# Kernel tuning notes

Hardware: AMD Instinct MI355X
Metric: run time of the kernel (lower is better)

## Reference

```python
import jax, jax.numpy as jnp
import numpy as np

N = 50000      # nodes
E = 1000000    # edges
D = 64         # in_dim == out_dim
R = 200        # num_rels


def setup_inputs() -> dict:
    key = jax.random.key(0)
    ks = jax.random.split(key, 11)
    return {
        "n_feats": jax.random.normal(ks[0], (N, D), jnp.float32),
        "r_feats": jax.random.normal(ks[1], (R, D), jnp.float32),
        "W_I_w": jax.random.normal(ks[2], (D, D), jnp.float32) * 0.1,
        "W_I_b": jax.random.normal(ks[3], (D,), jnp.float32) * 0.1,
        "W_O_w": jax.random.normal(ks[4], (D, D), jnp.float32) * 0.1,
        "W_O_b": jax.random.normal(ks[5], (D,), jnp.float32) * 0.1,
        "W_R_w": jax.random.normal(ks[6], (D, D), jnp.float32) * 0.1,
        "W_R_b": jax.random.normal(ks[7], (D,), jnp.float32) * 0.1,
        "src": jax.random.randint(ks[8], (E,), 0, N),
        "dst": jax.random.randint(ks[9], (E,), 0, N),
        "etype": jax.random.randint(ks[10], (E,), 0, R),
        "num_rels": R,
    }


def reference(n_feats, r_feats, W_I_w, W_I_b, W_O_w, W_O_b, W_R_w, W_R_b,
              src, dst, etype, num_rels):
    # per-edge composition (comp_fn='sub'): h_src - r[etype]   [E, D]
    comp_h = n_feats[src] - r_feats[etype]
    # conditional linear per edge: W_I for etype < num_rels//2, else W_O
    h_i = comp_h @ W_I_w.T + W_I_b
    h_o = comp_h @ W_O_w.T + W_O_b
    mask = (etype < num_rels // 2)[:, None]
    new_comp_h = jnp.where(mask, h_i, h_o)
    # segment-mean scatter to destination nodes (DGL fn.mean)
    num_nodes = n_feats.shape[0]
    seg_sum = jax.ops.segment_sum(new_comp_h, dst, num_segments=num_nodes)
    deg = jax.ops.segment_sum(jnp.ones((new_comp_h.shape[0],), new_comp_h.dtype),
                              dst, num_segments=num_nodes)
    n_out_feats = seg_sum / jnp.maximum(deg, 1.0)[:, None]
    # dropout in eval mode = identity; no batchnorm, no activation, no self-loop
    r_out_feats = r_feats @ W_R_w.T + W_R_b
    return n_out_feats, r_out_feats
```

## Files before the change

kernel.cpp:

```cpp
#include <hip/hip_runtime.h>


#define DIM 64
#define NPB 8
#define WPAD 68
#define NBUCK 256
#define EPB 4096
#define CAP 8192

__device__ __forceinline__ unsigned int pack_bf16(float2 v) {
    unsigned int a = __float_as_uint(v.x);
    unsigned int b = __float_as_uint(v.y);
    a = (a + 0x7FFFu + ((a >> 16) & 1u)) >> 16;
    b = (b + 0x7FFFu + ((b >> 16) & 1u)) >> 16;
    return (a & 0xFFFFu) | (b << 16);
}

__global__ __launch_bounds__(256) void cvt_kernel(
    const float* __restrict__ n_feats, const float* __restrict__ r_feats,
    unsigned int* __restrict__ nfb, unsigned int* __restrict__ rfb,
    int nN2, int nR2)
{
    int i = blockIdx.x * blockDim.x + threadIdx.x;
    if (i < nN2) {
        nfb[i] = pack_bf16(((const float2*)n_feats)[i]);
    } else if (i < nN2 + nR2) {
        int k = i - nN2;
        rfb[k] = pack_bf16(((const float2*)r_feats)[k]);
    }
}

__global__ __launch_bounds__(512) void scatter_kernel(
    const int* __restrict__ src, const int* __restrict__ dst,
    const int* __restrict__ etype, int* __restrict__ bcur,
    unsigned int* __restrict__ es, int E)
{
    __shared__ int cnt[NBUCK];
    __shared__ int loff[NBUCK];
    __shared__ int woff[NBUCK];
    __shared__ int lold[NBUCK];
    __shared__ unsigned int stg[EPB];

    int tid = threadIdx.x;
    int base = blockIdx.x * EPB;
    int end = min(base + EPB, E);
    int m = end - base;

    if (tid < NBUCK) cnt[tid] = 0;
    __syncthreads();

    unsigned int val[8];
    int bk[8];
    #pragma unroll
    for (int k = 0; k < 8; ++k) {
        int e = base + tid + k * 512;
        if (e < end) {
            unsigned int d = (unsigned)dst[e];
            bk[k] = (int)(d >> 8);
            val[k] = ((d & 255u) << 24) | (((unsigned)src[e]) << 8)
                   | (unsigned)etype[e];
            atomicAdd(&cnt[bk[k]], 1);
        } else {
            bk[k] = -1;
            val[k] = 0u;
        }
    }
    __syncthreads();

    if (tid < NBUCK) loff[tid] = cnt[tid];
    __syncthreads();
    for (int off = 1; off < NBUCK; off <<= 1) {
        int t = 0;
        if (tid < NBUCK && tid >= off) t = loff[tid - off];
        __syncthreads();
        if (tid < NBUCK) loff[tid] += t;
        __syncthreads();
    }
    if (tid < NBUCK) {
        int excl = loff[tid] - cnt[tid];
        woff[tid] = excl;
        lold[tid] = (cnt[tid] > 0) ? atomicAdd(&bcur[tid], cnt[tid]) : 0;
    }
    __syncthreads();

    #pragma unroll
    for (int k = 0; k < 8; ++k) {
        if (bk[k] >= 0) {
            int p = atomicAdd(&woff[bk[k]], 1);
            stg[p] = val[k];
        }
    }
    __syncthreads();

    for (int j = tid; j < m; j += 512) {
        int lo_ = 0, hi_ = NBUCK;
        while (lo_ < hi_) {
            int mid = (lo_ + hi_) >> 1;
            if (loff[mid] > j) hi_ = mid; else lo_ = mid + 1;
        }
        int b = lo_;
        int excl = loff[b] - cnt[b];
        int local = lold[b] + (j - excl);
        if (local < CAP) es[(size_t)b * CAP + local] = stg[j];
    }
}

__global__ __launch_bounds__(512) void bsort_kernel(
    const unsigned int* __restrict__ es, const int* __restrict__ bcur,
    unsigned int* __restrict__ es2, int* __restrict__ rowptr,
    int* __restrict__ deg, int* __restrict__ degI,
    const int* __restrict__ num_rels, int N)
{
    __shared__ int nd[512], nl[512], ncur[512];

    int b = blockIdx.x, tid = threadIdx.x;
    int base = b * CAP;
    int cnt = min(bcur[b], CAP);
    int half = num_rels[0] >> 1;

    nd[tid] = 0;
    __syncthreads();
    for (int j = tid; j < cnt; j += 512) {
        unsigned int e = es[base + j];
        int k = (int)((e >> 24) << 1) | ((int)(e & 0xFFu) >= half ? 1 : 0);
        atomicAdd(&nd[k], 1);
    }
    __syncthreads();

    nl[tid] = nd[tid];
    __syncthreads();
    for (int off = 1; off < 512; off <<= 1) {
        int t = (tid >= off) ? nl[tid - off] : 0;
        __syncthreads();
        nl[tid] += t;
        __syncthreads();
    }
    ncur[tid] = nl[tid] - nd[tid];
    if ((tid & 1) == 0) {
        int v = (b << 8) + (tid >> 1);
        if (v < N) {
            rowptr[v] = base + (nl[tid] - nd[tid]);
            degI[v]   = nd[tid];
            deg[v]    = nd[tid] + nd[tid + 1];
        }
    }
    __syncthreads();

    for (int j = tid; j < cnt; j += 512) {
        unsigned int e = es[base + j];
        int k = (int)((e >> 24) << 1) | ((int)(e & 0xFFu) >= half ? 1 : 0);
        int p = atomicAdd(&ncur[k], 1);
        es2[base + p] = e;
    }
}

__device__ __forceinline__ void acc8(const uint4 f, const uint4 r, float* a) {
    a[0] += __uint_as_float(f.x << 16)         - __uint_as_float(r.x << 16);
    a[1] += __uint_as_float(f.x & 0xFFFF0000u) - __uint_as_float(r.x & 0xFFFF0000u);
    a[2] += __uint_as_float(f.y << 16)         - __uint_as_float(r.y << 16);
    a[3] += __uint_as_float(f.y & 0xFFFF0000u) - __uint_as_float(r.y & 0xFFFF0000u);
    a[4] += __uint_as_float(f.z << 16)         - __uint_as_float(r.z << 16);
    a[5] += __uint_as_float(f.z & 0xFFFF0000u) - __uint_as_float(r.z & 0xFFFF0000u);
    a[6] += __uint_as_float(f.w << 16)         - __uint_as_float(r.w << 16);
    a[7] += __uint_as_float(f.w & 0xFFFF0000u) - __uint_as_float(r.w & 0xFFFF0000u);
}

#define EDGE_LOOP(BND, A)                                              \
    for (; i + 8 < (BND); i += 16) {                                   \
        unsigned int ea = es2[i], eb = es2[i + 8];                     \
        uint4 fa = nf4[(size_t)((ea >> 8) & 0xFFFFu) * 8 + fl];        \
        uint4 ra = rf4[(size_t)(ea & 0xFFu) * 8 + fl];                 \
        uint4 fb = nf4[(size_t)((eb >> 8) & 0xFFFFu) * 8 + fl];        \
        uint4 rb = rf4[(size_t)(eb & 0xFFu) * 8 + fl];                 \
        acc8(fa, ra, A);                                               \
        acc8(fb, rb, A);                                               \
    }                                                                  \
    for (; i < (BND); i += 8) {                                        \
        unsigned int ea = es2[i];                                      \
        uint4 fa = nf4[(size_t)((ea >> 8) & 0xFFFFu) * 8 + fl];        \
        uint4 ra = rf4[(size_t)(ea & 0xFFu) * 8 + fl];                 \
        acc8(fa, ra, A);                                               \
    }

__global__ __launch_bounds__(512, 4) void rows_kernel(
    const unsigned int* __restrict__ nfb, const unsigned int* __restrict__ rfb,
    const float* __restrict__ r_feats,
    const int* __restrict__ rowptr, const int* __restrict__ degs,
    const int* __restrict__ degIs, const unsigned int* __restrict__ es2,
    const float* __restrict__ W_I_w, const float* __restrict__ W_I_b,
    const float* __restrict__ W_O_w, const float* __restrict__ W_O_b,
    const float* __restrict__ W_R_w, const float* __restrict__ W_R_b,
    float* __restrict__ n_out, float* __restrict__ r_out, int N, int Rr)
{
    __shared__ float WIp[DIM * WPAD];
    __shared__ float WOp[DIM * WPAD];
    __shared__ float xI[NPB][DIM];
    __shared__ float xO[NPB][DIM];

    const int tid = threadIdx.x;
    for (int i = tid; i < DIM * DIM; i += 512) {
        int j = i >> 6, d = i & 63;
        WIp[j * WPAD + d] = W_I_w[i];
        WOp[j * WPAD + d] = W_O_w[i];
    }
    __syncthreads();

    const int wv = tid >> 6, lane = tid & 63;
    const int e8 = lane >> 3, fl = lane & 7;
    const uint4* nf4 = (const uint4*)nfb;
    const uint4* rf4 = (const uint4*)rfb;

    int row = blockIdx.x * NPB + wv;
    if (row < N) {
        int lo = rowptr[row];
        int dI = degIs[row];
        int dT = degs[row];
        int mid = lo + dI, hi = lo + dT;
        float aI[8] = {0.f, 0.f, 0.f, 0.f, 0.f, 0.f, 0.f, 0.f};
        float aO[8] = {0.f, 0.f, 0.f, 0.f, 0.f, 0.f, 0.f, 0.f};

        int i = lo + e8;
        EDGE_LOOP(mid, aI);
        i = mid + e8;
        EDGE_LOOP(hi, aO);

        #pragma unroll
        for (int d = 8; d < 64; d <<= 1) {
            #pragma unroll
            for (int k = 0; k < 8; ++k) {
                aI[k] += __shfl_xor(aI[k], d, 64);
                aO[k] += __shfl_xor(aO[k], d, 64);
            }
        }
        if (e8 == 0) {
            #pragma unroll
            for (int k = 0; k < 8; ++k) {
                xI[wv][fl * 8 + k] = aI[k];
                xO[wv][fl * 8 + k] = aO[k];
            }
        }

        float sum = (float)dI * W_I_b[lane] + (float)(dT - dI) * W_O_b[lane];
        #pragma unroll
        for (int d4 = 0; d4 < DIM; d4 += 4) {
            float4 wi = *(const float4*)&WIp[lane * WPAD + d4];
            float4 wo = *(const float4*)&WOp[lane * WPAD + d4];
            float4 xi = *(const float4*)&xI[wv][d4];
            float4 xo = *(const float4*)&xO[wv][d4];
            sum += wi.x*xi.x + wi.y*xi.y + wi.z*xi.z + wi.w*xi.w
                 + wo.x*xo.x + wo.y*xo.y + wo.z*xo.z + wo.w*xo.w;
        }
        __builtin_nontemporal_store(sum / (float)(dT > 1 ? dT : 1),
                                    &n_out[(size_t)row * DIM + lane]);
    } else if (row < N + Rr) {
        int r = row - N;
        const float4* wr4 = (const float4*)W_R_w;
        const float4* rr4 = (const float4*)r_feats;
        float sum = W_R_b[lane];
        #pragma unroll
        for (int d4 = 0; d4 < 16; ++d4) {
            float4 w = wr4[(size_t)lane * 16 + d4];
            float4 x = rr4[(size_t)r * 16 + d4];
            sum += w.x*x.x + w.y*x.y + w.z*x.z + w.w*x.w;
        }
        __builtin_nontemporal_store(sum, &r_out[(size_t)r * DIM + lane]);
    }
}

extern "C" void kernel_launch(void* const* d_in, const int* in_sizes, int n_in,
                              void* d_out, int out_size, void* d_ws, size_t ws_size,
                              hipStream_t stream) {
    const float* n_feats  = (const float*)d_in[0];
    const float* r_feats  = (const float*)d_in[1];
    const float* W_I_w    = (const float*)d_in[2];
    const float* W_I_b    = (const float*)d_in[3];
    const float* W_O_w    = (const float*)d_in[4];
    const float* W_O_b    = (const float*)d_in[5];
    const float* W_R_w    = (const float*)d_in[6];
    const float* W_R_b    = (const float*)d_in[7];
    const int*   src      = (const int*)d_in[8];
    const int*   dst      = (const int*)d_in[9];
    const int*   etype    = (const int*)d_in[10];
    const int*   num_rels = (const int*)d_in[11];

    const int N  = in_sizes[0] / DIM;
    const int Rr = in_sizes[1] / DIM;
    const int E  = in_sizes[8];

    unsigned int* es   = (unsigned int*)d_ws;
    unsigned int* es2  = es + (size_t)NBUCK * CAP;
    unsigned int* nfb  = es2 + (size_t)NBUCK * CAP;
    unsigned int* rfb  = nfb + (size_t)N * (DIM / 2);
    int* bcur   = (int*)(rfb + (size_t)Rr * (DIM / 2));
    int* rowptr = bcur + NBUCK;
    int* deg    = rowptr + N;
    int* degI   = deg + N;

    float* n_out = (float*)d_out;
    float* r_out = n_out + (size_t)N * DIM;

    hipMemsetAsync(bcur, 0, NBUCK * sizeof(int), stream);

    int nN2 = N * (DIM / 2), nR2 = Rr * (DIM / 2);
    cvt_kernel<<<(nN2 + nR2 + 255) / 256, 256, 0, stream>>>(
        n_feats, r_feats, nfb, rfb, nN2, nR2);

    int sb = (E + EPB - 1) / EPB;
    scatter_kernel<<<sb, 512, 0, stream>>>(src, dst, etype, bcur, es, E);

    int nbUsed = (N + 255) >> 8;
    bsort_kernel<<<nbUsed, 512, 0, stream>>>(
        es, bcur, es2, rowptr, deg, degI, num_rels, N);

    int rowsBlocks = (N + Rr + NPB - 1) / NPB;
    rows_kernel<<<rowsBlocks, 512, 0, stream>>>(
        nfb, rfb, r_feats, rowptr, deg, degI, es2,
        W_I_w, W_I_b, W_O_w, W_O_b, W_R_w, W_R_b,
        n_out, r_out, N, Rr);
}
```

Baseline: 192.9 us.

## Fuse conversion into scatter launch, stage bucket in LDS, merge I/O edge loops

The bf16 conversion kernel is folded into the scatter kernel as extra blocks, so one launch covers both and the two independent jobs can overlap. The bucket sort now loads each bucket into shared memory once instead of reading global memory twice. The rows kernel replaces its two separate edge loops (I half and O half) with one loop that keeps a total sum and a masked I sum, then derives the O sum as the difference. This removes per-row loop overhead and the tail imbalance, but adds an FMA per element, and the subtraction can change rounding. The conversion blocks also carry the scatter kernel's large shared-memory footprint, which may lower their occupancy.

```diff
diff --git a/kernel.cpp b/kernel.cpp
--- a/kernel.cpp
+++ b/kernel.cpp
@@ -16,24 +16,13 @@
     return (a & 0xFFFFu) | (b << 16);
 }
 
-__global__ __launch_bounds__(256) void cvt_kernel(
+__global__ __launch_bounds__(512) void build_kernel(
+    const int* __restrict__ src, const int* __restrict__ dst,
+    const int* __restrict__ etype, int* __restrict__ bcur,
+    unsigned int* __restrict__ es, int E, int sb,
     const float* __restrict__ n_feats, const float* __restrict__ r_feats,
     unsigned int* __restrict__ nfb, unsigned int* __restrict__ rfb,
     int nN2, int nR2)
-{
-    int i = blockIdx.x * blockDim.x + threadIdx.x;
-    if (i < nN2) {
-        nfb[i] = pack_bf16(((const float2*)n_feats)[i]);
-    } else if (i < nN2 + nR2) {
-        int k = i - nN2;
-        rfb[k] = pack_bf16(((const float2*)r_feats)[k]);
-    }
-}
-
-__global__ __launch_bounds__(512) void scatter_kernel(
-    const int* __restrict__ src, const int* __restrict__ dst,
-    const int* __restrict__ etype, int* __restrict__ bcur,
-    unsigned int* __restrict__ es, int E)
 {
     __shared__ int cnt[NBUCK];
     __shared__ int loff[NBUCK];
@@ -42,6 +31,18 @@
     __shared__ unsigned int stg[EPB];
 
     int tid = threadIdx.x;
+
+    if (blockIdx.x >= sb) {
+        int i = (blockIdx.x - sb) * 512 + tid;
+        if (i < nN2) {
+            nfb[i] = pack_bf16(((const float2*)n_feats)[i]);
+        } else if (i < nN2 + nR2) {
+            int k = i - nN2;
+            rfb[k] = pack_bf16(((const float2*)r_feats)[k]);
+        }
+        return;
+    }
+
     int base = blockIdx.x * EPB;
     int end = min(base + EPB, E);
     int m = end - base;
@@ -111,6 +112,7 @@
     int* __restrict__ deg, int* __restrict__ degI,
     const int* __restrict__ num_rels, int N)
 {
+    __shared__ unsigned int st[CAP];
     __shared__ int nd[512], nl[512], ncur[512];
 
     int b = blockIdx.x, tid = threadIdx.x;
@@ -119,9 +121,11 @@
     int half = num_rels[0] >> 1;
 
     nd[tid] = 0;
-    __syncthreads();
+    for (int j = tid; j < cnt; j += 512) st[j] = es[base + j];
+    __syncthreads();
+
     for (int j = tid; j < cnt; j += 512) {
-        unsigned int e = es[base + j];
+        unsigned int e = st[j];
         int k = (int)((e >> 24) << 1) | ((int)(e & 0xFFu) >= half ? 1 : 0);
         atomicAdd(&nd[k], 1);
     }
@@ -147,40 +151,33 @@
     __syncthreads();
 
     for (int j = tid; j < cnt; j += 512) {
-        unsigned int e = es[base + j];
+        unsigned int e = st[j];
         int k = (int)((e >> 24) << 1) | ((int)(e & 0xFFu) >= half ? 1 : 0);
         int p = atomicAdd(&ncur[k], 1);
         es2[base + p] = e;
     }
 }
 
-__device__ __forceinline__ void acc8(const uint4 f, const uint4 r, float* a) {
-    a[0] += __uint_as_float(f.x << 16)         - __uint_as_float(r.x << 16);
-    a[1] += __uint_as_float(f.x & 0xFFFF0000u) - __uint_as_float(r.x & 0xFFFF0000u);
-    a[2] += __uint_as_float(f.y << 16)         - __uint_as_float(r.y << 16);
-    a[3] += __uint_as_float(f.y & 0xFFFF0000u) - __uint_as_float(r.y & 0xFFFF0000u);
-    a[4] += __uint_as_float(f.z << 16)         - __uint_as_float(r.z << 16);
-    a[5] += __uint_as_float(f.z & 0xFFFF0000u) - __uint_as_float(r.z & 0xFFFF0000u);
-    a[6] += __uint_as_float(f.w << 16)         - __uint_as_float(r.w << 16);
-    a[7] += __uint_as_float(f.w & 0xFFFF0000u) - __uint_as_float(r.w & 0xFFFF0000u);
-}
-
-#define EDGE_LOOP(BND, A)                                              \
-    for (; i + 8 < (BND); i += 16) {                                   \
-        unsigned int ea = es2[i], eb = es2[i + 8];                     \
-        uint4 fa = nf4[(size_t)((ea >> 8) & 0xFFFFu) * 8 + fl];        \
-        uint4 ra = rf4[(size_t)(ea & 0xFFu) * 8 + fl];                 \
-        uint4 fb = nf4[(size_t)((eb >> 8) & 0xFFFFu) * 8 + fl];        \
-        uint4 rb = rf4[(size_t)(eb & 0xFFu) * 8 + fl];                 \
-        acc8(fa, ra, A);                                               \
-        acc8(fb, rb, A);                                               \
-    }                                                                  \
-    for (; i < (BND); i += 8) {                                        \
-        unsigned int ea = es2[i];                                      \
-        uint4 fa = nf4[(size_t)((ea >> 8) & 0xFFFFu) * 8 + fl];        \
-        uint4 ra = rf4[(size_t)(ea & 0xFFu) * 8 + fl];                 \
-        acc8(fa, ra, A);                                               \
-    }
+__device__ __forceinline__ void acc8m(const uint4 f, const uint4 r, float w,
+                                      float* aT, float* aI) {
+    float c;
+    c = __uint_as_float(f.x << 16)         - __uint_as_float(r.x << 16);
+    aT[0] += c; aI[0] = fmaf(w, c, aI[0]);
+    c = __uint_as_float(f.x & 0xFFFF0000u) - __uint_as_float(r.x & 0xFFFF0000u);
+    aT[1] += c; aI[1] = fmaf(w, c, aI[1]);
+    c = __uint_as_float(f.y << 16)         - __uint_as_float(r.y << 16);
+    aT[2] += c; aI[2] = fmaf(w, c, aI[2]);
+    c = __uint_as_float(f.y & 0xFFFF0000u) - __uint_as_float(r.y & 0xFFFF0000u);
+    aT[3] += c; aI[3] = fmaf(w, c, aI[3]);
+    c = __uint_as_float(f.z << 16)         - __uint_as_float(r.z << 16);
+    aT[4] += c; aI[4] = fmaf(w, c, aI[4]);
+    c = __uint_as_float(f.z & 0xFFFF0000u) - __uint_as_float(r.z & 0xFFFF0000u);
+    aT[5] += c; aI[5] = fmaf(w, c, aI[5]);
+    c = __uint_as_float(f.w << 16)         - __uint_as_float(r.w << 16);
+    aT[6] += c; aI[6] = fmaf(w, c, aI[6]);
+    c = __uint_as_float(f.w & 0xFFFF0000u) - __uint_as_float(r.w & 0xFFFF0000u);
+    aT[7] += c; aI[7] = fmaf(w, c, aI[7]);
+}
 
 __global__ __launch_bounds__(512, 4) void rows_kernel(
     const unsigned int* __restrict__ nfb, const unsigned int* __restrict__ rfb,
@@ -217,26 +214,41 @@
         int dT = degs[row];
         int mid = lo + dI, hi = lo + dT;
         float aI[8] = {0.f, 0.f, 0.f, 0.f, 0.f, 0.f, 0.f, 0.f};
-        float aO[8] = {0.f, 0.f, 0.f, 0.f, 0.f, 0.f, 0.f, 0.f};
+        float aT[8] = {0.f, 0.f, 0.f, 0.f, 0.f, 0.f, 0.f, 0.f};
 
         int i = lo + e8;
-        EDGE_LOOP(mid, aI);
-        i = mid + e8;
-        EDGE_LOOP(hi, aO);
+        for (; i + 8 < hi; i += 16) {
+            unsigned int ea = es2[i], eb = es2[i + 8];
+            uint4 fa = nf4[(size_t)((ea >> 8) & 0xFFFFu) * 8 + fl];
+            uint4 ra = rf4[(size_t)(ea & 0xFFu) * 8 + fl];
+            uint4 fb = nf4[(size_t)((eb >> 8) & 0xFFFFu) * 8 + fl];
+            uint4 rb = rf4[(size_t)(eb & 0xFFu) * 8 + fl];
+            float wa = (i < mid) ? 1.0f : 0.0f;
+            float wb = (i + 8 < mid) ? 1.0f : 0.0f;
+            acc8m(fa, ra, wa, aT, aI);
+            acc8m(fb, rb, wb, aT, aI);
+        }
+        for (; i < hi; i += 8) {
+            unsigned int ea = es2[i];
+            uint4 fa = nf4[(size_t)((ea >> 8) & 0xFFFFu) * 8 + fl];
+            uint4 ra = rf4[(size_t)(ea & 0xFFu) * 8 + fl];
+            float wa = (i < mid) ? 1.0f : 0.0f;
+            acc8m(fa, ra, wa, aT, aI);
+        }
 
         #pragma unroll
         for (int d = 8; d < 64; d <<= 1) {
             #pragma unroll
             for (int k = 0; k < 8; ++k) {
+                aT[k] += __shfl_xor(aT[k], d, 64);
                 aI[k] += __shfl_xor(aI[k], d, 64);
-                aO[k] += __shfl_xor(aO[k], d, 64);
             }
         }
         if (e8 == 0) {
             #pragma unroll
             for (int k = 0; k < 8; ++k) {
                 xI[wv][fl * 8 + k] = aI[k];
-                xO[wv][fl * 8 + k] = aO[k];
+                xO[wv][fl * 8 + k] = aT[k] - aI[k];
             }
         }
 
@@ -302,11 +314,11 @@
     hipMemsetAsync(bcur, 0, NBUCK * sizeof(int), stream);
 
     int nN2 = N * (DIM / 2), nR2 = Rr * (DIM / 2);
-    cvt_kernel<<<(nN2 + nR2 + 255) / 256, 256, 0, stream>>>(
+    int sb = (E + EPB - 1) / EPB;
+    int cvtB = (nN2 + nR2 + 511) / 512;
+    build_kernel<<<sb + cvtB, 512, 0, stream>>>(
+        src, dst, etype, bcur, es, E, sb,
         n_feats, r_feats, nfb, rfb, nN2, nR2);
-
-    int sb = (E + EPB - 1) / EPB;
-    scatter_kernel<<<sb, 512, 0, stream>>>(src, dst, etype, bcur, es, E);
 
     int nbUsed = (N + 255) >> 8;
     bsort_kernel<<<nbUsed, 512, 0, stream>>>(
```

New measurement: 186.8 us. 3.2% less time.
